# Optimization experiments

Hardware: AMD Instinct MI355X
Metric: run time of the kernel (lower is better)

Reference implementation:

```python
import jax, jax.numpy as jnp
import numpy as np

# Dims: B docs, L tokens, D hidden, H heads, NE padded entities (min_height),
# M mentions per entity, P entity pairs per doc, BLK bilinear block, NL labels.
B, L, D, H, NE, M, P = 4, 1024, 768, 12, 42, 4, 512
BLK, NL = 64, 97
OFFSET = 1  # self.offset = 1 (CLS token shift)


def setup_inputs() -> dict:
    key = jax.random.key(0)
    ks = jax.random.split(key, 10)
    sequence_output = jax.random.normal(ks[0], (B, L, D), jnp.float32)
    att = jax.random.uniform(ks[1], (B, H, L, L), jnp.float32)
    attention = att / att.sum(-1, keepdims=True)  # row-stochastic like softmax attn
    mention_pos = jax.random.randint(ks[2], (B, NE, M), 0, 1000, dtype=jnp.int32)
    hts = jax.random.randint(ks[3], (B, P, 2), 0, NE, dtype=jnp.int32)
    W_head = jax.random.normal(ks[4], (2 * D, D), jnp.float32) * 0.02
    b_head = jnp.zeros((D,), jnp.float32)
    W_tail = jax.random.normal(ks[5], (2 * D, D), jnp.float32) * 0.02
    b_tail = jnp.zeros((D,), jnp.float32)
    W_bi = jax.random.normal(ks[6], (D * BLK, NL), jnp.float32) * 0.02
    b_bi = jnp.zeros((NL,), jnp.float32)
    return dict(sequence_output=sequence_output, attention=attention,
                mention_pos=mention_pos, hts=hts,
                W_head=W_head, b_head=b_head, W_tail=W_tail, b_tail=b_tail,
                W_bi=W_bi, b_bi=b_bi)


def reference(sequence_output, attention, mention_pos, hts,
              W_head, b_head, W_tail, b_tail, W_bi, b_bi):
    pos = mention_pos + OFFSET                               # [B,NE,M]
    # --- get_hrt: entity embeds = logsumexp over mention start tokens ---
    e_emb = jax.vmap(lambda s, p: s[p])(sequence_output, pos)    # [B,NE,M,D]
    entity_embs = jax.nn.logsumexp(e_emb, axis=2)                # [B,NE,D]
    # entity attention = mean over mentions of attn rows           [B,NE,H,L]
    e_att = jax.vmap(lambda a, p: a[:, p])(attention, pos)       # [B,H,NE,M,L]
    entity_atts = e_att.mean(3).transpose(0, 2, 1, 3)            # [B,NE,H,L]
    # --- get_channel_map: ht_att = (h_att * t_att).mean(heads), normalized ---
    ht_att = jnp.einsum('bihl,bjhl->bijl', entity_atts, entity_atts) / H  # [B,NE,NE,L]
    ht_att = ht_att / (ht_att.sum(-1, keepdims=True) + 1e-5)
    rs_map = jnp.einsum('bijl,bld->bijd', ht_att, sequence_output)        # [B,NE,NE,D]
    # --- gather head/tail entity embeds and pooled context per pair ---
    h_idx, t_idx = hts[..., 0], hts[..., 1]                      # [B,P]
    hs = jnp.take_along_axis(entity_embs, h_idx[..., None], axis=1)  # [B,P,D]
    ts = jnp.take_along_axis(entity_embs, t_idx[..., None], axis=1)  # [B,P,D]
    rs = jax.vmap(lambda m, h, t: m[h, t])(rs_map, h_idx, t_idx)     # [B,P,D]
    # --- extractors + grouped bilinear classifier ---
    zs = jnp.tanh(jnp.concatenate([hs, rs], -1) @ W_head + b_head)   # [B,P,D]
    zo = jnp.tanh(jnp.concatenate([ts, rs], -1) @ W_tail + b_tail)   # [B,P,D]
    b1 = zs.reshape(B, P, D // BLK, BLK)
    b2 = zo.reshape(B, P, D // BLK, BLK)
    bl = (b1[..., :, None] * b2[..., None, :]).reshape(B, P, D * BLK)
    logits = bl @ W_bi + b_bi                                        # [B,P,NL]
    return logits
```

## Files before the change

kernel.cpp:

```cpp
#include <hip/hip_runtime.h>

constexpr int Bc = 4, Lc = 1024, Dc = 768, Hc = 12, NEc = 42, Mc = 4, Pc = 512, NLc = 97;
constexpr int BE   = Bc * NEc;
constexpr int BEp  = 176;
constexpr int ROWS = Bc * Pc;
constexpr int N2   = 2 * Dc;

typedef __attribute__((ext_vector_type(8))) short short8;
typedef _Float16 half8 __attribute__((ext_vector_type(8)));
typedef __attribute__((ext_vector_type(4))) float f32x4;

__device__ __forceinline__ f32x4 mfma_bf(short8 a, short8 b, f32x4 c) {
    return __builtin_amdgcn_mfma_f32_16x16x32_bf16(a, b, c, 0, 0, 0);
}
__device__ __forceinline__ f32x4 mfma_h(half8 a, half8 b, f32x4 c) {
    return __builtin_amdgcn_mfma_f32_16x16x32_f16(a, b, c, 0, 0, 0);
}
__device__ __forceinline__ unsigned short f2bf(float x) {
    unsigned int u = __float_as_uint(x);
    return (unsigned short)((u + 0x7fffu + ((u >> 16) & 1u)) >> 16);
}
__device__ __forceinline__ float bf2f(unsigned short h) {
    return __uint_as_float(((unsigned int)h) << 16);
}
__device__ __forceinline__ short8 ld8(const unsigned short* p) {
    return *(const short8*)(const void*)p;
}
__device__ __forceinline__ half8 ldh8(const _Float16* p) {
    return *(const half8*)(const void*)p;
}


__global__ __launch_bounds__(256) void k_embs(const float* __restrict__ seq,
                                              const int* __restrict__ mpos,
                                              unsigned short* __restrict__ ep) {
    int be = blockIdx.x, mt = be >> 4, lm = be & 15;
    float vals[3] = {0.f, 0.f, 0.f};
    if (be < BE) {
        int b = be / NEc;
        const int* pp = mpos + be * Mc;
        int p0 = pp[0] + 1, p1 = pp[1] + 1, p2 = pp[2] + 1, p3 = pp[3] + 1;
        const float* s = seq + (size_t)b * Lc * Dc;
        #pragma unroll
        for (int i = 0; i < 3; ++i) {
            int d = threadIdx.x + i * 256;
            float x0 = s[(size_t)p0 * Dc + d], x1 = s[(size_t)p1 * Dc + d];
            float x2 = s[(size_t)p2 * Dc + d], x3 = s[(size_t)p3 * Dc + d];
            float mx = fmaxf(fmaxf(x0, x1), fmaxf(x2, x3));
            vals[i] = mx + logf(expf(x0 - mx) + expf(x1 - mx) + expf(x2 - mx) + expf(x3 - mx));
        }
    }
    #pragma unroll
    for (int i = 0; i < 3; ++i) {
        int d = threadIdx.x + i * 256;
        int idx = ((mt * 24 + (d >> 5)) << 9) + (((d >> 3) & 3) << 7) + (lm << 3) + (d & 7);
        ep[idx] = f2bf(vals[i]);
    }
}

__global__ __launch_bounds__(256) void k_eatt(const float* __restrict__ att,
                                              const int* __restrict__ mpos,
                                              unsigned short* __restrict__ eatt) {
    int be = blockIdx.x, h = blockIdx.y, b = be / NEc;
    const int* pp = mpos + be * Mc;
    const float* a = att + ((size_t)(b * Hc + h)) * Lc * Lc;
    const float4* r0 = (const float4*)(a + (size_t)(pp[0] + 1) * Lc);
    const float4* r1 = (const float4*)(a + (size_t)(pp[1] + 1) * Lc);
    const float4* r2 = (const float4*)(a + (size_t)(pp[2] + 1) * Lc);
    const float4* r3 = (const float4*)(a + (size_t)(pp[3] + 1) * Lc);
    unsigned short* o = eatt + ((size_t)be * Hc + h) * Lc;
    int t = threadIdx.x;
    float4 v0 = r0[t], v1 = r1[t], v2 = r2[t], v3 = r3[t];
    o[t * 4 + 0] = f2bf(0.25f * (v0.x + v1.x + v2.x + v3.x));
    o[t * 4 + 1] = f2bf(0.25f * (v0.y + v1.y + v2.y + v3.y));
    o[t * 4 + 2] = f2bf(0.25f * (v0.z + v1.z + v2.z + v3.z));
    o[t * 4 + 3] = f2bf(0.25f * (v0.w + v1.w + v2.w + v3.w));
}

__global__ __launch_bounds__(256) void k_pairw(const unsigned short* __restrict__ eatt,
                                               const int* __restrict__ hts,
                                               unsigned short* __restrict__ pwp) {
    int bp = blockIdx.x, b = bp / Pc;
    int hi = hts[bp * 2], ti = hts[bp * 2 + 1];
    const unsigned short* ai = eatt + ((size_t)(b * NEc + hi)) * Hc * Lc;
    const unsigned short* aj = eatt + ((size_t)(b * NEc + ti)) * Hc * Lc;
    int l0 = threadIdx.x * 4;
    float acc[4] = {0.f, 0.f, 0.f, 0.f};
    #pragma unroll
    for (int h = 0; h < Hc; ++h) {
        uint2 ua = *(const uint2*)(ai + h * Lc + l0);
        uint2 ub = *(const uint2*)(aj + h * Lc + l0);
        acc[0] += bf2f(ua.x & 0xffff) * bf2f(ub.x & 0xffff);
        acc[1] += bf2f(ua.x >> 16)    * bf2f(ub.x >> 16);
        acc[2] += bf2f(ua.y & 0xffff) * bf2f(ub.y & 0xffff);
        acc[3] += bf2f(ua.y >> 16)    * bf2f(ub.y >> 16);
    }
    float lsum = acc[0] + acc[1] + acc[2] + acc[3];
    #pragma unroll
    for (int off = 32; off > 0; off >>= 1) lsum += __shfl_down(lsum, off, 64);
    __shared__ float red[4];
    __shared__ float sinv;
    int lane = threadIdx.x & 63, wv = threadIdx.x >> 6;
    if (lane == 0) red[wv] = lsum;
    __syncthreads();
    if (threadIdx.x == 0) sinv = 1.f / (red[0] + red[1] + red[2] + red[3] + 1.2e-4f);
    __syncthreads();
    float s = sinv;
    unsigned short w0 = f2bf(acc[0] * s), w1 = f2bf(acc[1] * s);
    unsigned short w2 = f2bf(acc[2] * s), w3 = f2bf(acc[3] * s);
    int mt = bp >> 4, lm = bp & 15, kb = l0 >> 5, quad = (l0 >> 3) & 3, j0 = l0 & 7;
    unsigned short* dst = pwp + ((mt * 32 + kb) << 9) + (quad << 7) + (lm << 3) + j0;
    *(uint2*)dst = make_uint2((unsigned)w0 | ((unsigned)w1 << 16),
                              (unsigned)w2 | ((unsigned)w3 << 16));
}

__global__ __launch_bounds__(256) void k_tr_seq(const float* __restrict__ seq,
                                                unsigned short* __restrict__ sp) {
    __shared__ float tile[64][65];
    int l0 = blockIdx.x * 64, d0 = blockIdx.y * 64, b = blockIdx.z;
    int t = threadIdx.x;
    const float* s = seq + (size_t)b * Lc * Dc;
    #pragma unroll
    for (int i = 0; i < 16; ++i) {
        int idx = t + i * 256, r = idx >> 6, c = idx & 63;
        tile[r][c] = s[(size_t)(l0 + r) * Dc + d0 + c];
    }
    __syncthreads();
    unsigned short* outb = sp + (size_t)b * 48 * 32 * 512;
    int flat = t * 2, lane = flat >> 3, j = flat & 7;
    #pragma unroll
    for (int nt_i = 0; nt_i < 4; ++nt_i)
        #pragma unroll
        for (int kb_i = 0; kb_i < 2; ++kb_i) {
            int kl = kb_i * 32 + (lane >> 4) * 8 + j;
            int c  = nt_i * 16 + (lane & 15);
            unsigned int v = (unsigned)f2bf(tile[kl][c]) | ((unsigned)f2bf(tile[kl + 1][c]) << 16);
            *(unsigned int*)&outb[(((d0 / 16 + nt_i) * 32 + (l0 / 32 + kb_i)) << 9) + flat] = v;
        }
}

__global__ __launch_bounds__(256) void k_tr_w(const float* __restrict__ Wh,
                                              const float* __restrict__ Wt,
                                              unsigned short* __restrict__ wp1,
                                              unsigned short* __restrict__ wp2) {
    __shared__ float tile[64][65];
    int k0 = blockIdx.x * 64, n0 = blockIdx.y * 64, which = blockIdx.z;
    const float* W = which ? Wt : Wh;
    int t = threadIdx.x;
    #pragma unroll
    for (int i = 0; i < 16; ++i) {
        int idx = t + i * 256, r = idx >> 6, c = idx & 63;
        tile[r][c] = W[(size_t)(k0 + r) * Dc + n0 + c];
    }
    __syncthreads();
    unsigned short* dst = (k0 < Dc) ? wp1 : wp2;
    int kb0 = ((k0 < Dc) ? k0 : (k0 - Dc)) / 32;
    int nt0 = which * 48 + n0 / 16;
    int flat = t * 2, lane = flat >> 3, j = flat & 7;
    #pragma unroll
    for (int nt_i = 0; nt_i < 4; ++nt_i)
        #pragma unroll
        for (int kb_i = 0; kb_i < 2; ++kb_i) {
            int kl = kb_i * 32 + (lane >> 4) * 8 + j;
            int c  = nt_i * 16 + (lane & 15);
            unsigned int v = (unsigned)f2bf(tile[kl][c]) | ((unsigned)f2bf(tile[kl + 1][c]) << 16);
            *(unsigned int*)&dst[(((nt0 + nt_i) * 24 + kb0 + kb_i) << 9) + flat] = v;
        }
}

__global__ __launch_bounds__(256) void k_tr_wbi(const float* __restrict__ wbi,
                                                _Float16* __restrict__ wbp) {
    __shared__ float lds[64 * 97];
    int x = blockIdx.x, g = blockIdx.y;
    const float* src = wbi + (size_t)(g * 4096 + x * 64) * NLc;
    for (int i = threadIdx.x; i < 64 * NLc; i += 256) lds[i] = src[i];
    __syncthreads();
    int flat = threadIdx.x * 2, lane = flat >> 3, j = flat & 7;
    int lm = lane & 15, qj = (lane >> 4) * 8 + j;
    #pragma unroll
    for (int nt = 0; nt < 7; ++nt)
        #pragma unroll
        for (int half = 0; half < 2; ++half) {
            int y = half * 32 + qj;
            int n = nt * 16 + lm;
            _Float16 v0 = (n < NLc) ? (_Float16)lds[y * NLc + n] : (_Float16)0.f;
            _Float16 v1 = (n < NLc) ? (_Float16)lds[(y + 1) * NLc + n] : (_Float16)0.f;
            size_t base = ((((size_t)(nt * 12 + g) * 64 + x) * 2 + half) << 9);
            _Float16* d = wbp + base + flat;
            d[0] = v0; d[1] = v1;
        }
}

__global__ __launch_bounds__(256) void k_rs(const unsigned short* __restrict__ pwp,
                                            const unsigned short* __restrict__ sp,
                                            unsigned short* __restrict__ rsp) {
    int tid = threadIdx.x, wave = tid >> 6, lane = tid & 63;
    int quad = lane >> 4, lm = lane & 15;
    int nt = blockIdx.y * 4 + wave, b = blockIdx.z, mb = blockIdx.x;
    int mt0 = b * 32 + mb * 4;
    const unsigned short* bbase = sp + (((size_t)b * 48 + nt) * 32 << 9) + lane * 8;
    const unsigned short* abase = pwp + ((size_t)mt0 * 32 << 9) + lane * 8;
    f32x4 acc[4] = {};
    for (int kb = 0; kb < 32; ++kb) {
        short8 bf = ld8(bbase + kb * 512);
        #pragma unroll
        for (int mf = 0; mf < 4; ++mf)
            acc[mf] = mfma_bf(ld8(abase + (mf * 32 + kb) * 512), bf, acc[mf]);
    }
    int n = nt * 16 + lm, kbo = n >> 5, lq = ((n >> 3) & 3) << 4, jo = n & 7;
    #pragma unroll
    for (int mf = 0; mf < 4; ++mf) {
        unsigned short* db = rsp + (((mt0 + mf) * 24 + kbo) << 9) + jo;
        #pragma unroll
        for (int r = 0; r < 4; ++r)
            db[(lq + quad * 4 + r) << 3] = f2bf(acc[mf][r]);
    }
}

__global__ __launch_bounds__(256) void k_E(const unsigned short* __restrict__ ep,
                                           const unsigned short* __restrict__ wp1,
                                           unsigned short* __restrict__ E) {
    int tid = threadIdx.x, wave = tid >> 6, lane = tid & 63;
    int quad = lane >> 4, lm = lane & 15;
    int mt = blockIdx.x, nt = blockIdx.y * 4 + wave;
    const unsigned short* ab = ep + (mt * 24 << 9) + lane * 8;
    const unsigned short* bb = wp1 + (nt * 24 << 9) + lane * 8;
    f32x4 acc = {};
    for (int kb = 0; kb < 24; ++kb)
        acc = mfma_bf(ld8(ab + kb * 512), ld8(bb + kb * 512), acc);
    #pragma unroll
    for (int r = 0; r < 4; ++r)
        E[(size_t)(mt * 16 + quad * 4 + r) * N2 + nt * 16 + lm] = f2bf(acc[r]);
}

__global__ __launch_bounds__(256) void k_R(const unsigned short* __restrict__ rsp,
                                           const unsigned short* __restrict__ wp2,
                                           unsigned short* __restrict__ R) {
    int tid = threadIdx.x, wave = tid >> 6, lane = tid & 63;
    int quad = lane >> 4, lm = lane & 15;
    int mt0 = blockIdx.x * 4, nt = blockIdx.y * 4 + wave;
    const unsigned short* bb = wp2 + (nt * 24 << 9) + lane * 8;
    const unsigned short* ab = rsp + ((size_t)mt0 * 24 << 9) + lane * 8;
    f32x4 acc[4] = {};
    for (int kb = 0; kb < 24; ++kb) {
        short8 bf = ld8(bb + kb * 512);
        #pragma unroll
        for (int mf = 0; mf < 4; ++mf)
            acc[mf] = mfma_bf(ld8(ab + (mf * 24 + kb) * 512), bf, acc[mf]);
    }
    #pragma unroll
    for (int mf = 0; mf < 4; ++mf)
        #pragma unroll
        for (int r = 0; r < 4; ++r)
            R[(size_t)((mt0 + mf) * 16 + quad * 4 + r) * N2 + nt * 16 + lm] = f2bf(acc[mf][r]);
}

__global__ __launch_bounds__(256) void k_zfin(const unsigned short* __restrict__ E,
                                              const unsigned short* __restrict__ R,
                                              const int* __restrict__ hts,
                                              const float* __restrict__ bh,
                                              const float* __restrict__ bt,
                                              _Float16* __restrict__ zs,
                                              _Float16* __restrict__ zop) {
    int row = blockIdx.x, b = row >> 9;
    int hh = hts[row * 2], tt = hts[row * 2 + 1];
    const unsigned short* Eh = E + (size_t)(b * NEc + hh) * N2;
    const unsigned short* Et = E + (size_t)(b * NEc + tt) * N2 + Dc;
    const unsigned short* Rr = R + (size_t)row * N2;
    #pragma unroll
    for (int i = 0; i < 3; ++i) {
        int n = threadIdx.x + i * 256;
        float vs = tanhf(bf2f(Eh[n]) + bf2f(Rr[n]) + bh[n]);
        float vo = tanhf(bf2f(Et[n]) + bf2f(Rr[Dc + n]) + bt[n]);
        zs[(size_t)row * Dc + n] = (_Float16)vs;
        int idx = (((row >> 4) * 24 + (n >> 5)) << 9) + (((((n >> 3) & 3) << 4) + (row & 15)) << 3) + (n & 7);
        zop[idx] = (_Float16)vo;
    }
}

__global__ __launch_bounds__(256) void k_bilin(const _Float16* __restrict__ zs,
                                               const _Float16* __restrict__ zop,
                                               const _Float16* __restrict__ wbp,
                                               const float* __restrict__ bbi,
                                               float* __restrict__ out) {
    __shared__ _Float16 zlds[256 * 72];
    int tid = threadIdx.x, wave = tid >> 6, lane = tid & 63;
    int quad = lane >> 4, lm = lane & 15;
    int pb = blockIdx.x, nt = blockIdx.y, g = blockIdx.z;
    {
        const half8* src = (const half8*)(zs + ((size_t)(pb * 256 + tid)) * Dc + g * 64);
        half8* dst = (half8*)&zlds[tid * 72];
        #pragma unroll
        for (int c = 0; c < 8; ++c) dst[c] = src[c];
    }
    __syncthreads();
    int mt0 = pb * 16 + wave * 4;
    half8 zofr[4][2];
    #pragma unroll
    for (int mf = 0; mf < 4; ++mf)
        #pragma unroll
        for (int hf = 0; hf < 2; ++hf)
            zofr[mf][hf] = ldh8(zop + (((mt0 + mf) * 24 + g * 2 + hf) << 9) + lane * 8);
    const _Float16* wbase = wbp + ((size_t)(nt * 12 + g) << 16) + lane * 8;
    const _Float16* zrow = &zlds[(wave * 64 + lm) * 72];
    f32x4 acc[4] = {};
    for (int x = 0; x < 64; ++x) {
        half8 b0 = ldh8(wbase + x * 1024);
        half8 b1 = ldh8(wbase + x * 1024 + 512);
        #pragma unroll
        for (int mf = 0; mf < 4; ++mf) {
            _Float16 s = zrow[mf * 16 * 72 + x];
            half8 bc = {s, s, s, s, s, s, s, s};
            acc[mf] = mfma_h(bc * zofr[mf][0], b0, acc[mf]);
            acc[mf] = mfma_h(bc * zofr[mf][1], b1, acc[mf]);
        }
    }
    int n = nt * 16 + lm;
    if (n < NLc) {
        #pragma unroll
        for (int mf = 0; mf < 4; ++mf)
            #pragma unroll
            for (int r = 0; r < 4; ++r) {
                int row = (mt0 + mf) * 16 + quad * 4 + r;
                float v = acc[mf][r];
                if (g == 0) v += bbi[n];
                atomicAdd(out + (size_t)row * NLc + n, v);
            }
    }
}

extern "C" void kernel_launch(void* const* d_in, const int* in_sizes, int n_in,
                              void* d_out, int out_size, void* d_ws, size_t ws_size,
                              hipStream_t stream) {
    const float* seq  = (const float*)d_in[0];
    const float* att  = (const float*)d_in[1];
    const int*   mpos = (const int*)d_in[2];
    const int*   hts  = (const int*)d_in[3];
    const float* Wh   = (const float*)d_in[4];
    const float* bh   = (const float*)d_in[5];
    const float* Wt   = (const float*)d_in[6];
    const float* bt   = (const float*)d_in[7];
    const float* Wbi  = (const float*)d_in[8];
    const float* bbi  = (const float*)d_in[9];
    float* out = (float*)d_out;

    char* w = (char*)d_ws;
    unsigned short* embs_p = (unsigned short*)(w);
    unsigned short* eatt_b = (unsigned short*)(w + 270336);
    unsigned short* pw_p   = (unsigned short*)(w + 4399104);
    unsigned short* seq_p  = (unsigned short*)(w + 8593408);
    _Float16*       wbi_p  = (_Float16*)(w);
    unsigned short* wp1    = (unsigned short*)(w + 14884864);
    unsigned short* wp2    = (unsigned short*)(w + 17244160);
    unsigned short* E      = (unsigned short*)(w + 19603456);
    unsigned short* rs_p   = (unsigned short*)(w + 20144128);
    unsigned short* R      = (unsigned short*)(w + 23289856);
    _Float16*       zs     = (_Float16*)(w + 29581312);
    _Float16*       zo_p   = (_Float16*)(w + 32727040);

    hipMemsetAsync(d_out, 0, (size_t)out_size * sizeof(float), stream);

    k_embs  <<<BEp, 256, 0, stream>>>(seq, mpos, embs_p);
    k_eatt  <<<dim3(BE, Hc), 256, 0, stream>>>(att, mpos, eatt_b);
    k_pairw <<<ROWS, 256, 0, stream>>>(eatt_b, hts, pw_p);
    k_tr_seq<<<dim3(16, 12, 4), 256, 0, stream>>>(seq, seq_p);
    k_tr_w  <<<dim3(24, 12, 2), 256, 0, stream>>>(Wh, Wt, wp1, wp2);
    k_rs    <<<dim3(8, 12, 4), 256, 0, stream>>>(pw_p, seq_p, rs_p);
    k_E     <<<dim3(11, 24), 256, 0, stream>>>(embs_p, wp1, E);
    k_tr_wbi<<<dim3(64, 12), 256, 0, stream>>>(Wbi, wbi_p);
    k_R     <<<dim3(32, 24), 256, 0, stream>>>(rs_p, wp2, R);
    k_zfin  <<<ROWS, 256, 0, stream>>>(E, R, hts, bh, bt, zs, zo_p);
    k_bilin <<<dim3(8, 7, 12), 256, 0, stream>>>(zs, zo_p, wbi_p, bbi, out);
}
```

Before: 387.6 us.

## Merge preprocessing kernels and output zeroing into one launch; fuse rs and E GEMMs

Combines entity embedding, entity attention gather, sequence/weight transposes, bilinear-weight repacking and output zeroing into a single block-dispatched kernel, and merges the rs and E GEMMs into one launch. Moves the bilinear weight buffer to its own workspace region so it no longer aliases the early buffers. The aim is to cut launch overhead and the gaps between small dependent launches. The cost is that every prep block reserves the largest shared-memory footprint, which may reduce occupancy for the gather-heavy blocks.

```diff
diff --git a/kernel.cpp b/kernel.cpp
--- a/kernel.cpp
+++ b/kernel.cpp
@@ -31,50 +31,144 @@
 }
 
 
-__global__ __launch_bounds__(256) void k_embs(const float* __restrict__ seq,
+constexpr int PB_EMBS  = 0;
+constexpr int PB_EATT  = PB_EMBS + BEp;
+constexpr int PB_TRSEQ = PB_EATT + BE * Hc;
+constexpr int PB_TRW   = PB_TRSEQ + 768;
+constexpr int PB_TRWBI = PB_TRW + 576;
+constexpr int PB_ZERO  = PB_TRWBI + 768;
+constexpr int PB_TOTAL = PB_ZERO + 97;
+
+__global__ __launch_bounds__(256) void k_prep(const float* __restrict__ seq,
+                                              const float* __restrict__ att,
                                               const int* __restrict__ mpos,
-                                              unsigned short* __restrict__ ep) {
-    int be = blockIdx.x, mt = be >> 4, lm = be & 15;
-    float vals[3] = {0.f, 0.f, 0.f};
-    if (be < BE) {
-        int b = be / NEc;
+                                              const float* __restrict__ Wh,
+                                              const float* __restrict__ Wt,
+                                              const float* __restrict__ wbi,
+                                              unsigned short* __restrict__ ep,
+                                              unsigned short* __restrict__ eatt,
+                                              unsigned short* __restrict__ sp,
+                                              unsigned short* __restrict__ wp1,
+                                              unsigned short* __restrict__ wp2,
+                                              _Float16* __restrict__ wbp,
+                                              float* __restrict__ out_zero) {
+    __shared__ float smem[64 * 97];
+    int blk = blockIdx.x;
+    int t = threadIdx.x;
+
+    if (blk < PB_EATT) {
+        int be = blk - PB_EMBS, mt = be >> 4, lm = be & 15;
+        float vals[3] = {0.f, 0.f, 0.f};
+        if (be < BE) {
+            int b = be / NEc;
+            const int* pp = mpos + be * Mc;
+            int p0 = pp[0] + 1, p1 = pp[1] + 1, p2 = pp[2] + 1, p3 = pp[3] + 1;
+            const float* s = seq + (size_t)b * Lc * Dc;
+            #pragma unroll
+            for (int i = 0; i < 3; ++i) {
+                int d = t + i * 256;
+                float x0 = s[(size_t)p0 * Dc + d], x1 = s[(size_t)p1 * Dc + d];
+                float x2 = s[(size_t)p2 * Dc + d], x3 = s[(size_t)p3 * Dc + d];
+                float mx = fmaxf(fmaxf(x0, x1), fmaxf(x2, x3));
+                vals[i] = mx + logf(expf(x0 - mx) + expf(x1 - mx) + expf(x2 - mx) + expf(x3 - mx));
+            }
+        }
+        #pragma unroll
+        for (int i = 0; i < 3; ++i) {
+            int d = t + i * 256;
+            int idx = ((mt * 24 + (d >> 5)) << 9) + (((d >> 3) & 3) << 7) + (lm << 3) + (d & 7);
+            ep[idx] = f2bf(vals[i]);
+        }
+    } else if (blk < PB_TRSEQ) {
+        int idx = blk - PB_EATT;
+        int be = idx / Hc, h = idx - be * Hc, b = be / NEc;
         const int* pp = mpos + be * Mc;
-        int p0 = pp[0] + 1, p1 = pp[1] + 1, p2 = pp[2] + 1, p3 = pp[3] + 1;
+        const float* a = att + ((size_t)(b * Hc + h)) * Lc * Lc;
+        const float4* r0 = (const float4*)(a + (size_t)(pp[0] + 1) * Lc);
+        const float4* r1 = (const float4*)(a + (size_t)(pp[1] + 1) * Lc);
+        const float4* r2 = (const float4*)(a + (size_t)(pp[2] + 1) * Lc);
+        const float4* r3 = (const float4*)(a + (size_t)(pp[3] + 1) * Lc);
+        unsigned short* o = eatt + ((size_t)be * Hc + h) * Lc;
+        float4 v0 = r0[t], v1 = r1[t], v2 = r2[t], v3 = r3[t];
+        o[t * 4 + 0] = f2bf(0.25f * (v0.x + v1.x + v2.x + v3.x));
+        o[t * 4 + 1] = f2bf(0.25f * (v0.y + v1.y + v2.y + v3.y));
+        o[t * 4 + 2] = f2bf(0.25f * (v0.z + v1.z + v2.z + v3.z));
+        o[t * 4 + 3] = f2bf(0.25f * (v0.w + v1.w + v2.w + v3.w));
+    } else if (blk < PB_TRW) {
+        int idx = blk - PB_TRSEQ;
+        int xb = idx & 15, yb = (idx >> 4) % 12, b = idx / 192;
+        int l0 = xb * 64, d0 = yb * 64;
         const float* s = seq + (size_t)b * Lc * Dc;
         #pragma unroll
-        for (int i = 0; i < 3; ++i) {
-            int d = threadIdx.x + i * 256;
-            float x0 = s[(size_t)p0 * Dc + d], x1 = s[(size_t)p1 * Dc + d];
-            float x2 = s[(size_t)p2 * Dc + d], x3 = s[(size_t)p3 * Dc + d];
-            float mx = fmaxf(fmaxf(x0, x1), fmaxf(x2, x3));
-            vals[i] = mx + logf(expf(x0 - mx) + expf(x1 - mx) + expf(x2 - mx) + expf(x3 - mx));
-        }
-    }
-    #pragma unroll
-    for (int i = 0; i < 3; ++i) {
-        int d = threadIdx.x + i * 256;
-        int idx = ((mt * 24 + (d >> 5)) << 9) + (((d >> 3) & 3) << 7) + (lm << 3) + (d & 7);
-        ep[idx] = f2bf(vals[i]);
-    }
-}
-
-__global__ __launch_bounds__(256) void k_eatt(const float* __restrict__ att,
-                                              const int* __restrict__ mpos,
-                                              unsigned short* __restrict__ eatt) {
-    int be = blockIdx.x, h = blockIdx.y, b = be / NEc;
-    const int* pp = mpos + be * Mc;
-    const float* a = att + ((size_t)(b * Hc + h)) * Lc * Lc;
-    const float4* r0 = (const float4*)(a + (size_t)(pp[0] + 1) * Lc);
-    const float4* r1 = (const float4*)(a + (size_t)(pp[1] + 1) * Lc);
-    const float4* r2 = (const float4*)(a + (size_t)(pp[2] + 1) * Lc);
-    const float4* r3 = (const float4*)(a + (size_t)(pp[3] + 1) * Lc);
-    unsigned short* o = eatt + ((size_t)be * Hc + h) * Lc;
-    int t = threadIdx.x;
-    float4 v0 = r0[t], v1 = r1[t], v2 = r2[t], v3 = r3[t];
-    o[t * 4 + 0] = f2bf(0.25f * (v0.x + v1.x + v2.x + v3.x));
-    o[t * 4 + 1] = f2bf(0.25f * (v0.y + v1.y + v2.y + v3.y));
-    o[t * 4 + 2] = f2bf(0.25f * (v0.z + v1.z + v2.z + v3.z));
-    o[t * 4 + 3] = f2bf(0.25f * (v0.w + v1.w + v2.w + v3.w));
+        for (int i = 0; i < 16; ++i) {
+            int ii = t + i * 256, r = ii >> 6, c = ii & 63;
+            smem[r * 65 + c] = s[(size_t)(l0 + r) * Dc + d0 + c];
+        }
+        __syncthreads();
+        unsigned short* outb = sp + (size_t)b * 48 * 32 * 512;
+        int flat = t * 2, lane = flat >> 3, j = flat & 7;
+        #pragma unroll
+        for (int nt_i = 0; nt_i < 4; ++nt_i)
+            #pragma unroll
+            for (int kb_i = 0; kb_i < 2; ++kb_i) {
+                int kl = kb_i * 32 + (lane >> 4) * 8 + j;
+                int c  = nt_i * 16 + (lane & 15);
+                unsigned int v = (unsigned)f2bf(smem[kl * 65 + c]) |
+                                 ((unsigned)f2bf(smem[(kl + 1) * 65 + c]) << 16);
+                *(unsigned int*)&outb[(((d0 / 16 + nt_i) * 32 + (l0 / 32 + kb_i)) << 9) + flat] = v;
+            }
+    } else if (blk < PB_TRWBI) {
+        int idx = blk - PB_TRW;
+        int xb = idx % 24, yb = (idx / 24) % 12, which = idx / 288;
+        int k0 = xb * 64, n0 = yb * 64;
+        const float* W = which ? Wt : Wh;
+        #pragma unroll
+        for (int i = 0; i < 16; ++i) {
+            int ii = t + i * 256, r = ii >> 6, c = ii & 63;
+            smem[r * 65 + c] = W[(size_t)(k0 + r) * Dc + n0 + c];
+        }
+        __syncthreads();
+        unsigned short* dst = (k0 < Dc) ? wp1 : wp2;
+        int kb0 = ((k0 < Dc) ? k0 : (k0 - Dc)) / 32;
+        int nt0 = which * 48 + n0 / 16;
+        int flat = t * 2, lane = flat >> 3, j = flat & 7;
+        #pragma unroll
+        for (int nt_i = 0; nt_i < 4; ++nt_i)
+            #pragma unroll
+            for (int kb_i = 0; kb_i < 2; ++kb_i) {
+                int kl = kb_i * 32 + (lane >> 4) * 8 + j;
+                int c  = nt_i * 16 + (lane & 15);
+                unsigned int v = (unsigned)f2bf(smem[kl * 65 + c]) |
+                                 ((unsigned)f2bf(smem[(kl + 1) * 65 + c]) << 16);
+                *(unsigned int*)&dst[(((nt0 + nt_i) * 24 + kb0 + kb_i) << 9) + flat] = v;
+            }
+    } else if (blk < PB_ZERO) {
+        int idx = blk - PB_TRWBI;
+        int x = idx & 63, g = idx >> 6;
+        const float* src = wbi + (size_t)(g * 4096 + x * 64) * NLc;
+        for (int i = t; i < 64 * NLc; i += 256) smem[i] = src[i];
+        __syncthreads();
+        int flat = t * 2, lane = flat >> 3, j = flat & 7;
+        int lm = lane & 15, qj = (lane >> 4) * 8 + j;
+        #pragma unroll
+        for (int nt = 0; nt < 7; ++nt)
+            #pragma unroll
+            for (int half = 0; half < 2; ++half) {
+                int y = half * 32 + qj;
+                int n = nt * 16 + lm;
+                _Float16 v0 = (n < NLc) ? (_Float16)smem[y * NLc + n] : (_Float16)0.f;
+                _Float16 v1 = (n < NLc) ? (_Float16)smem[(y + 1) * NLc + n] : (_Float16)0.f;
+                size_t base = ((((size_t)(nt * 12 + g) * 64 + x) * 2 + half) << 9);
+                _Float16* d = wbp + base + flat;
+                d[0] = v0; d[1] = v1;
+            }
+    } else {
+        int idx = blk - PB_ZERO;
+        float4* o = (float4*)(out_zero + (size_t)idx * 2048);
+        float4 z = {0.f, 0.f, 0.f, 0.f};
+        o[t] = z;
+        o[t + 256] = z;
+    }
 }
 
 __global__ __launch_bounds__(256) void k_pairw(const unsigned short* __restrict__ eatt,
@@ -114,123 +208,49 @@
                               (unsigned)w2 | ((unsigned)w3 << 16));
 }
 
-__global__ __launch_bounds__(256) void k_tr_seq(const float* __restrict__ seq,
-                                                unsigned short* __restrict__ sp) {
-    __shared__ float tile[64][65];
-    int l0 = blockIdx.x * 64, d0 = blockIdx.y * 64, b = blockIdx.z;
-    int t = threadIdx.x;
-    const float* s = seq + (size_t)b * Lc * Dc;
-    #pragma unroll
-    for (int i = 0; i < 16; ++i) {
-        int idx = t + i * 256, r = idx >> 6, c = idx & 63;
-        tile[r][c] = s[(size_t)(l0 + r) * Dc + d0 + c];
-    }
-    __syncthreads();
-    unsigned short* outb = sp + (size_t)b * 48 * 32 * 512;
-    int flat = t * 2, lane = flat >> 3, j = flat & 7;
-    #pragma unroll
-    for (int nt_i = 0; nt_i < 4; ++nt_i)
-        #pragma unroll
-        for (int kb_i = 0; kb_i < 2; ++kb_i) {
-            int kl = kb_i * 32 + (lane >> 4) * 8 + j;
-            int c  = nt_i * 16 + (lane & 15);
-            unsigned int v = (unsigned)f2bf(tile[kl][c]) | ((unsigned)f2bf(tile[kl + 1][c]) << 16);
-            *(unsigned int*)&outb[(((d0 / 16 + nt_i) * 32 + (l0 / 32 + kb_i)) << 9) + flat] = v;
-        }
-}
-
-__global__ __launch_bounds__(256) void k_tr_w(const float* __restrict__ Wh,
-                                              const float* __restrict__ Wt,
-                                              unsigned short* __restrict__ wp1,
-                                              unsigned short* __restrict__ wp2) {
-    __shared__ float tile[64][65];
-    int k0 = blockIdx.x * 64, n0 = blockIdx.y * 64, which = blockIdx.z;
-    const float* W = which ? Wt : Wh;
-    int t = threadIdx.x;
-    #pragma unroll
-    for (int i = 0; i < 16; ++i) {
-        int idx = t + i * 256, r = idx >> 6, c = idx & 63;
-        tile[r][c] = W[(size_t)(k0 + r) * Dc + n0 + c];
-    }
-    __syncthreads();
-    unsigned short* dst = (k0 < Dc) ? wp1 : wp2;
-    int kb0 = ((k0 < Dc) ? k0 : (k0 - Dc)) / 32;
-    int nt0 = which * 48 + n0 / 16;
-    int flat = t * 2, lane = flat >> 3, j = flat & 7;
-    #pragma unroll
-    for (int nt_i = 0; nt_i < 4; ++nt_i)
-        #pragma unroll
-        for (int kb_i = 0; kb_i < 2; ++kb_i) {
-            int kl = kb_i * 32 + (lane >> 4) * 8 + j;
-            int c  = nt_i * 16 + (lane & 15);
-            unsigned int v = (unsigned)f2bf(tile[kl][c]) | ((unsigned)f2bf(tile[kl + 1][c]) << 16);
-            *(unsigned int*)&dst[(((nt0 + nt_i) * 24 + kb0 + kb_i) << 9) + flat] = v;
-        }
-}
-
-__global__ __launch_bounds__(256) void k_tr_wbi(const float* __restrict__ wbi,
-                                                _Float16* __restrict__ wbp) {
-    __shared__ float lds[64 * 97];
-    int x = blockIdx.x, g = blockIdx.y;
-    const float* src = wbi + (size_t)(g * 4096 + x * 64) * NLc;
-    for (int i = threadIdx.x; i < 64 * NLc; i += 256) lds[i] = src[i];
-    __syncthreads();
-    int flat = threadIdx.x * 2, lane = flat >> 3, j = flat & 7;
-    int lm = lane & 15, qj = (lane >> 4) * 8 + j;
-    #pragma unroll
-    for (int nt = 0; nt < 7; ++nt)
-        #pragma unroll
-        for (int half = 0; half < 2; ++half) {
-            int y = half * 32 + qj;
-            int n = nt * 16 + lm;
-            _Float16 v0 = (n < NLc) ? (_Float16)lds[y * NLc + n] : (_Float16)0.f;
-            _Float16 v1 = (n < NLc) ? (_Float16)lds[(y + 1) * NLc + n] : (_Float16)0.f;
-            size_t base = ((((size_t)(nt * 12 + g) * 64 + x) * 2 + half) << 9);
-            _Float16* d = wbp + base + flat;
-            d[0] = v0; d[1] = v1;
-        }
-}
-
-__global__ __launch_bounds__(256) void k_rs(const unsigned short* __restrict__ pwp,
-                                            const unsigned short* __restrict__ sp,
-                                            unsigned short* __restrict__ rsp) {
+__global__ __launch_bounds__(256) void k_rsE(const unsigned short* __restrict__ pwp,
+                                             const unsigned short* __restrict__ sp,
+                                             const unsigned short* __restrict__ ep,
+                                             const unsigned short* __restrict__ wp1,
+                                             unsigned short* __restrict__ rsp,
+                                             unsigned short* __restrict__ E) {
     int tid = threadIdx.x, wave = tid >> 6, lane = tid & 63;
     int quad = lane >> 4, lm = lane & 15;
-    int nt = blockIdx.y * 4 + wave, b = blockIdx.z, mb = blockIdx.x;
-    int mt0 = b * 32 + mb * 4;
-    const unsigned short* bbase = sp + (((size_t)b * 48 + nt) * 32 << 9) + lane * 8;
-    const unsigned short* abase = pwp + ((size_t)mt0 * 32 << 9) + lane * 8;
-    f32x4 acc[4] = {};
-    for (int kb = 0; kb < 32; ++kb) {
-        short8 bf = ld8(bbase + kb * 512);
-        #pragma unroll
-        for (int mf = 0; mf < 4; ++mf)
-            acc[mf] = mfma_bf(ld8(abase + (mf * 32 + kb) * 512), bf, acc[mf]);
-    }
-    int n = nt * 16 + lm, kbo = n >> 5, lq = ((n >> 3) & 3) << 4, jo = n & 7;
-    #pragma unroll
-    for (int mf = 0; mf < 4; ++mf) {
-        unsigned short* db = rsp + (((mt0 + mf) * 24 + kbo) << 9) + jo;
+    int blk = blockIdx.x;
+    if (blk < 384) {
+        int mb = blk & 7, ntq = (blk >> 3) % 12, b = blk / 96;
+        int nt = ntq * 4 + wave;
+        int mt0 = b * 32 + mb * 4;
+        const unsigned short* bbase = sp + (((size_t)b * 48 + nt) * 32 << 9) + lane * 8;
+        const unsigned short* abase = pwp + ((size_t)mt0 * 32 << 9) + lane * 8;
+        f32x4 acc[4] = {};
+        for (int kb = 0; kb < 32; ++kb) {
+            short8 bf = ld8(bbase + kb * 512);
+            #pragma unroll
+            for (int mf = 0; mf < 4; ++mf)
+                acc[mf] = mfma_bf(ld8(abase + (mf * 32 + kb) * 512), bf, acc[mf]);
+        }
+        int n = nt * 16 + lm, kbo = n >> 5, lq = ((n >> 3) & 3) << 4, jo = n & 7;
+        #pragma unroll
+        for (int mf = 0; mf < 4; ++mf) {
+            unsigned short* db = rsp + (((mt0 + mf) * 24 + kbo) << 9) + jo;
+            #pragma unroll
+            for (int r = 0; r < 4; ++r)
+                db[(lq + quad * 4 + r) << 3] = f2bf(acc[mf][r]);
+        }
+    } else {
+        int idx = blk - 384;
+        int mt = idx % 11, ntq = idx / 11;
+        int nt = ntq * 4 + wave;
+        const unsigned short* ab = ep + (mt * 24 << 9) + lane * 8;
+        const unsigned short* bb = wp1 + (nt * 24 << 9) + lane * 8;
+        f32x4 acc = {};
+        for (int kb = 0; kb < 24; ++kb)
+            acc = mfma_bf(ld8(ab + kb * 512), ld8(bb + kb * 512), acc);
         #pragma unroll
         for (int r = 0; r < 4; ++r)
-            db[(lq + quad * 4 + r) << 3] = f2bf(acc[mf][r]);
-    }
-}
-
-__global__ __launch_bounds__(256) void k_E(const unsigned short* __restrict__ ep,
-                                           const unsigned short* __restrict__ wp1,
-                                           unsigned short* __restrict__ E) {
-    int tid = threadIdx.x, wave = tid >> 6, lane = tid & 63;
-    int quad = lane >> 4, lm = lane & 15;
-    int mt = blockIdx.x, nt = blockIdx.y * 4 + wave;
-    const unsigned short* ab = ep + (mt * 24 << 9) + lane * 8;
-    const unsigned short* bb = wp1 + (nt * 24 << 9) + lane * 8;
-    f32x4 acc = {};
-    for (int kb = 0; kb < 24; ++kb)
-        acc = mfma_bf(ld8(ab + kb * 512), ld8(bb + kb * 512), acc);
-    #pragma unroll
-    for (int r = 0; r < 4; ++r)
-        E[(size_t)(mt * 16 + quad * 4 + r) * N2 + nt * 16 + lm] = f2bf(acc[r]);
+            E[(size_t)(mt * 16 + quad * 4 + r) * N2 + nt * 16 + lm] = f2bf(acc[r]);
+    }
 }
 
 __global__ __launch_bounds__(256) void k_R(const unsigned short* __restrict__ rsp,
@@ -349,26 +369,20 @@
     unsigned short* eatt_b = (unsigned short*)(w + 270336);
     unsigned short* pw_p   = (unsigned short*)(w + 4399104);
     unsigned short* seq_p  = (unsigned short*)(w + 8593408);
-    _Float16*       wbi_p  = (_Float16*)(w);
-    unsigned short* wp1    = (unsigned short*)(w + 14884864);
-    unsigned short* wp2    = (unsigned short*)(w + 17244160);
-    unsigned short* E      = (unsigned short*)(w + 19603456);
-    unsigned short* rs_p   = (unsigned short*)(w + 20144128);
-    unsigned short* R      = (unsigned short*)(w + 23289856);
-    _Float16*       zs     = (_Float16*)(w + 29581312);
-    _Float16*       zo_p   = (_Float16*)(w + 32727040);
-
-    hipMemsetAsync(d_out, 0, (size_t)out_size * sizeof(float), stream);
-
-    k_embs  <<<BEp, 256, 0, stream>>>(seq, mpos, embs_p);
-    k_eatt  <<<dim3(BE, Hc), 256, 0, stream>>>(att, mpos, eatt_b);
-    k_pairw <<<ROWS, 256, 0, stream>>>(eatt_b, hts, pw_p);
-    k_tr_seq<<<dim3(16, 12, 4), 256, 0, stream>>>(seq, seq_p);
-    k_tr_w  <<<dim3(24, 12, 2), 256, 0, stream>>>(Wh, Wt, wp1, wp2);
-    k_rs    <<<dim3(8, 12, 4), 256, 0, stream>>>(pw_p, seq_p, rs_p);
-    k_E     <<<dim3(11, 24), 256, 0, stream>>>(embs_p, wp1, E);
-    k_tr_wbi<<<dim3(64, 12), 256, 0, stream>>>(Wbi, wbi_p);
-    k_R     <<<dim3(32, 24), 256, 0, stream>>>(rs_p, wp2, R);
-    k_zfin  <<<ROWS, 256, 0, stream>>>(E, R, hts, bh, bt, zs, zo_p);
-    k_bilin <<<dim3(8, 7, 12), 256, 0, stream>>>(zs, zo_p, wbi_p, bbi, out);
-}
+    _Float16*       wbi_p  = (_Float16*)(w + 14884864);
+    unsigned short* wp1    = (unsigned short*)(w + 25894912);
+    unsigned short* wp2    = (unsigned short*)(w + 28254208);
+    unsigned short* E      = (unsigned short*)(w + 30613504);
+    unsigned short* rs_p   = (unsigned short*)(w + 31154176);
+    unsigned short* R      = (unsigned short*)(w + 34299904);
+    _Float16*       zs     = (_Float16*)(w + 40591360);
+    _Float16*       zo_p   = (_Float16*)(w + 43737088);
+
+    k_prep <<<PB_TOTAL, 256, 0, stream>>>(seq, att, mpos, Wh, Wt, Wbi,
+                                          embs_p, eatt_b, seq_p, wp1, wp2, wbi_p, out);
+    k_pairw<<<ROWS, 256, 0, stream>>>(eatt_b, hts, pw_p);
+    k_rsE  <<<648, 256, 0, stream>>>(pw_p, seq_p, embs_p, wp1, rs_p, E);
+    k_R    <<<dim3(32, 24), 256, 0, stream>>>(rs_p, wp2, R);
+    k_zfin <<<ROWS, 256, 0, stream>>>(E, R, hts, bh, bt, zs, zo_p);
+    k_bilin<<<dim3(8, 7, 12), 256, 0, stream>>>(zs, zo_p, wbi_p, bbi, out);
+}
```

After: 371.8 us. 4.1% less time.
